# Kernel tuning notes

Measured on AMD Instinct MI355X. Metric: run time of the kernel, lower is better.

Reference implementation:

```python
import jax, jax.numpy as jnp
import numpy as np

HEADS = 16
HEAD_DIM = 64
EMB = HEADS * HEAD_DIM
MAX_REL = 512
B, L = 4, 1024


def _rel_indices(length_q, length_k):
    # Shaw-style clipped relative distance indices into the embeddings table
    dist = jnp.arange(length_k)[None, :] - jnp.arange(length_q)[:, None]
    return jnp.clip(dist, -MAX_REL, MAX_REL) + MAX_REL  # [Lq, Lk] in [0, 2*MAX_REL]


def setup_inputs() -> dict:
    key = jax.random.key(0)
    ks = jax.random.split(key, 16)
    d = {
        "query": jax.random.normal(ks[0], (B, L, EMB), jnp.float32),
        "key": jax.random.normal(ks[1], (B, L, EMB), jnp.float32),
        "value": jax.random.normal(ks[2], (B, L, EMB), jnp.float32),
        "mask": jnp.ones((B, 1, L, L), jnp.int32),
        # per-head Linear(head_dims, head_dims) weights stored torch-style [out, in]
        "Wq": jax.random.normal(ks[3], (HEAD_DIM, HEAD_DIM), jnp.float32) / np.sqrt(HEAD_DIM),
        "bq": jax.random.normal(ks[4], (HEAD_DIM,), jnp.float32) * 0.02,
        "Wk": jax.random.normal(ks[5], (HEAD_DIM, HEAD_DIM), jnp.float32) / np.sqrt(HEAD_DIM),
        "bk": jax.random.normal(ks[6], (HEAD_DIM,), jnp.float32) * 0.02,
        "Wv": jax.random.normal(ks[7], (HEAD_DIM, HEAD_DIM), jnp.float32) / np.sqrt(HEAD_DIM),
        "bv": jax.random.normal(ks[8], (HEAD_DIM,), jnp.float32) * 0.02,
        "Wfc": jax.random.normal(ks[9], (EMB, EMB), jnp.float32) / np.sqrt(EMB),
        "bfc": jax.random.normal(ks[10], (EMB,), jnp.float32) * 0.02,
        "rel_k_table": jax.random.normal(ks[11], (2 * MAX_REL + 1, HEAD_DIM), jnp.float32) * 0.02,
        "rel_v_table": jax.random.normal(ks[12], (2 * MAX_REL + 1, HEAD_DIM), jnp.float32) * 0.02,
    }
    return d


def reference(query, key, value, mask, Wq, bq, Wk, bk, Wv, bv, Wfc, bfc, rel_k_table, rel_v_table):
    b, lq, _ = query.shape
    lk = key.shape[1]
    # split heads then per-head linear projections (torch Linear: x @ W.T + b)
    q = query.reshape(b, lq, HEADS, HEAD_DIM) @ Wq.T + bq
    k = key.reshape(b, lk, HEADS, HEAD_DIM) @ Wk.T + bk
    v = value.reshape(b, lk, HEADS, HEAD_DIM) @ Wv.T + bv

    score = jnp.einsum('bqhd,bkhd->bhqk', q, k)  # [B,H,Lq,Lk]
    score = jnp.where(mask == 0, jnp.float32(-1e20), score)

    idx = _rel_indices(lq, lk)
    a_key = rel_k_table[idx]    # [Lq, Lk, D]
    a_val = rel_v_table[idx]    # [Lq, Lk, D]
    score = score + jnp.einsum('blhd,lrd->bhlr', q, a_key)

    attn = jax.nn.softmax(score / np.sqrt(HEAD_DIM), axis=-1)

    out = jnp.einsum('bhqv,bvhd->bqhd', attn, v)
    # original: einsum('brhl,hld->bhrd', attn[b,h,q,k], a_val[q,k,d]) -> [b,q,h,d]
    out = out + jnp.einsum('bhql,qld->bqhd', attn, a_val)
    out = out.reshape(b, lq, EMB)
    return out @ Wfc.T + bfc
```

## Files before the change

kernel.cpp:

```cpp
#include <hip/hip_runtime.h>
#include <hip/hip_bf16.h>
#include <hip/hip_fp16.h>

#define SEQ 1024
#define HEADS 16
#define HDIM 64
#define EMB 1024
#define TQ 32
#define KQ 256
#define PBA_S 264
#define PBB_S 328
#define RELK_ROWS 1040
#define RELV_S 1064

typedef __bf16 bf16x8 __attribute__((ext_vector_type(8)));
typedef float floatx4 __attribute__((ext_vector_type(4)));

static __device__ __forceinline__ unsigned short f2bu(float f) {
    __bf16 h = (__bf16)f;
    return __builtin_bit_cast(unsigned short, h);
}
static __device__ __forceinline__ float b2f(unsigned short u) {
    unsigned v = ((unsigned)u) << 16;
    return __builtin_bit_cast(float, v);
}

__global__ __launch_bounds__(256) void sa_proj_kernel(
    const float* __restrict__ qin, const float* __restrict__ kin,
    const float* __restrict__ vin,
    const unsigned short* __restrict__ wqb, const unsigned short* __restrict__ wkb,
    const unsigned short* __restrict__ wvb,
    const float* __restrict__ bq, const float* __restrict__ bk,
    const float* __restrict__ bv_,
    unsigned short* __restrict__ qb, unsigned short* __restrict__ kb,
    unsigned short* __restrict__ vtb) {
    const int t = threadIdx.x;
    const int w = t >> 6, lane = t & 63;
    const int quad = lane >> 4, l16 = lane & 15;
    const int which = blockIdx.y;
    const int bx = blockIdx.x;
    const int r0 = (bx >> 2) * 16;
    const int h = (bx & 3) * 4 + w;
    const int bidx = r0 >> 10;
    const int l0 = r0 & 1023;
    const float* x = (which == 0) ? qin : (which == 1) ? kin : vin;
    const unsigned short* Wb = (which == 0) ? wqb : (which == 1) ? wkb : wvb;
    const float* bias = (which == 0) ? bq : (which == 1) ? bk : bv_;

    bf16x8 wf[4][2];
#pragma unroll
    for (int dt = 0; dt < 4; ++dt)
#pragma unroll
        for (int ks = 0; ks < 2; ++ks)
            wf[dt][ks] = *(const bf16x8*)(Wb + (size_t)(dt * 16 + l16) * 64 + ks * 32 + quad * 8);

    bf16x8 xf[2];
#pragma unroll
    for (int ks = 0; ks < 2; ++ks) {
        const float* xp = x + (size_t)(r0 + l16) * EMB + h * 64 + ks * 32 + quad * 8;
        float4 lo = *(const float4*)xp;
        float4 hi = *(const float4*)(xp + 4);
        unsigned short px[8];
        px[0] = f2bu(lo.x); px[1] = f2bu(lo.y); px[2] = f2bu(lo.z); px[3] = f2bu(lo.w);
        px[4] = f2bu(hi.x); px[5] = f2bu(hi.y); px[6] = f2bu(hi.z); px[7] = f2bu(hi.w);
        xf[ks] = *(bf16x8*)px;
    }
    const int bh = bidx * HEADS + h;

    if (which < 2) {
        float biasd[4];
#pragma unroll
        for (int dt = 0; dt < 4; ++dt) biasd[dt] = bias[dt * 16 + l16];
        const float sc = (which == 0) ? 0.125f : 1.0f;
        unsigned short* dst = (which == 0) ? qb : kb;
        floatx4 acc[4];
#pragma unroll
        for (int dt = 0; dt < 4; ++dt) acc[dt] = floatx4{0.f, 0.f, 0.f, 0.f};
#pragma unroll
        for (int dt = 0; dt < 4; ++dt)
#pragma unroll
            for (int ks = 0; ks < 2; ++ks)
                acc[dt] = __builtin_amdgcn_mfma_f32_16x16x32_bf16(xf[ks], wf[dt][ks], acc[dt], 0, 0, 0);
#pragma unroll
        for (int dt = 0; dt < 4; ++dt)
#pragma unroll
            for (int i = 0; i < 4; ++i) {
                const int lr = l0 + quad * 4 + i;
                float val = (acc[dt][i] + biasd[dt]) * sc;
                dst[((size_t)bh * SEQ + lr) * 64 + dt * 16 + l16] = f2bu(val);
            }
    } else {
        float biasv[4][4];
#pragma unroll
        for (int dt = 0; dt < 4; ++dt)
#pragma unroll
            for (int i = 0; i < 4; ++i) biasv[dt][i] = bias[dt * 16 + quad * 4 + i];
        floatx4 acc[4];
#pragma unroll
        for (int dt = 0; dt < 4; ++dt) acc[dt] = floatx4{0.f, 0.f, 0.f, 0.f};
#pragma unroll
        for (int dt = 0; dt < 4; ++dt)
#pragma unroll
            for (int ks = 0; ks < 2; ++ks)
                acc[dt] = __builtin_amdgcn_mfma_f32_16x16x32_bf16(wf[dt][ks], xf[ks], acc[dt], 0, 0, 0);
#pragma unroll
        for (int dt = 0; dt < 4; ++dt)
#pragma unroll
            for (int i = 0; i < 4; ++i) {
                const int d = dt * 16 + quad * 4 + i;
                float val = acc[dt][i] + biasv[dt][i];
                vtb[((size_t)bh * 64 + d) * SEQ + l0 + l16] = f2bu(val);
            }
    }
}

#define NW (1024 * 1024)
#define NRK (RELK_ROWS * 64)
#define NRV (64 * RELV_S)
#define NWP (3 * 4096)
#define CONV_BLOCKS ((NW + NRK + NRV + NWP) / 256)
__global__ __launch_bounds__(256) void sa_prep_kernel(
    const float* __restrict__ Wfc, const float* __restrict__ relk,
    const float* __restrict__ relv,
    const float* __restrict__ Wq, const float* __restrict__ Wk,
    const float* __restrict__ Wv, const int* __restrict__ mask,
    unsigned short* __restrict__ wfcb, unsigned short* __restrict__ relkb,
    unsigned short* __restrict__ relvtb,
    unsigned short* __restrict__ wqb, unsigned short* __restrict__ wkb,
    unsigned short* __restrict__ wvb, unsigned* __restrict__ part) {
    const int bx = blockIdx.x;
    const int t = threadIdx.x;
    if (bx < CONV_BLOCKS) {
        int i = bx * 256 + t;
        if (i < NW) {
            wfcb[i] = f2bu(Wfc[i]);
        } else if (i < NW + NRK) {
            int j = i - NW;
            int r = j >> 6, d = j & 63;
            relkb[j] = (r <= 1024) ? f2bu(relk[r * 64 + d]) : 0;
        } else if (i < NW + NRK + NRV) {
            int j = i - NW - NRK;
            int d = j / RELV_S, c = j - d * RELV_S;
            relvtb[j] = (c <= 1024) ? f2bu(relv[c * 64 + d]) : 0;
        } else {
            int j = i - NW - NRK - NRV;
            int which = j >> 12, e = j & 4095;
            const float* src = (which == 0) ? Wq : (which == 1) ? Wk : Wv;
            unsigned short* dst = (which == 0) ? wqb : (which == 1) ? wkb : wvb;
            dst[e] = f2bu(src[e]);
        }
    } else {
        const int mb = bx - CONV_BLOCKS;
        const int b = mb >> 6, chunk = mb & 63;
        const int4* p = (const int4*)(mask + (size_t)b * (SEQ * SEQ) + chunk * 16384);
        int ok = 1;
#pragma unroll
        for (int i = 0; i < 16; ++i) {
            int4 v = p[t + i * 256];
            ok &= (v.x != 0 && v.y != 0 && v.z != 0 && v.w != 0) ? 1 : 0;
        }
        unsigned long long bal = __ballot(ok);
        __shared__ unsigned wok[4];
        if ((t & 63) == 0) wok[t >> 6] = (bal == ~0ull) ? 1u : 0u;
        __syncthreads();
        if (t == 0)
            part[b * 64 + chunk] = (wok[0] & wok[1] & wok[2] & wok[3]) ? 0xFFFFFFFFu : 0u;
    }
}

__global__ void sa_maskred2(const unsigned* __restrict__ part, unsigned* __restrict__ flags) {
    int t = threadIdx.x;
    if (t < 4) {
        unsigned f = 0xFFFFFFFFu;
        for (int i = 0; i < 64; ++i) f &= part[t * 64 + i];
        flags[t] = f;
    }
}

__global__ __launch_bounds__(512, 8) void sa_attn_kernel(
    const unsigned short* __restrict__ qb, const unsigned short* __restrict__ kb,
    const unsigned short* __restrict__ vtb, const int* __restrict__ mask,
    const unsigned short* __restrict__ relkb, const unsigned short* __restrict__ relvtb,
    const unsigned* __restrict__ flags, __half* __restrict__ Opart,
    float2* __restrict__ ms) {
    __shared__ __align__(16) unsigned short PbA[TQ * PBA_S];
    __shared__ __align__(16) unsigned short PbB[TQ * PBB_S];
    __shared__ float wred[3][TQ * 8];

    const int tid = threadIdx.x;
    const int w = tid >> 6, lane = tid & 63;
    const int quad = lane >> 4, l16 = lane & 15;
    const int bid = blockIdx.x;
    const int quarter = bid & 3;
    const int qt = (bid >> 2) & 31;
    const int bh = bid >> 7;
    const int q0 = qt * TQ;
    const int k0 = quarter * KQ;
    const int b = bh >> 4;
    const bool mfull = (flags[b] == 0xFFFFFFFFu);

    const int cmin = min(512, max(-512, k0 - (q0 + 31))) + 512;
    const int cmax = min(512, max(-512, k0 + 255 - q0)) + 512;
    const int rsb = cmin & ~15;
    const int cb0 = cmin & ~7;

    bf16x8 aq[2][2];
#pragma unroll
    for (int rt = 0; rt < 2; ++rt) {
        const unsigned short* qrow = qb + ((size_t)bh * SEQ + q0 + rt * 16 + l16) * 64;
        aq[rt][0] = *(const bf16x8*)(qrow + quad * 8);
        aq[rt][1] = *(const bf16x8*)(qrow + 32 + quad * 8);
    }

    {
        const int ct_lo = cmin >> 4, ct_hi = cmax >> 4;
        for (int ct = ct_lo + w; ct <= ct_hi; ct += 8) {
            bf16x8 bf0 = *(const bf16x8*)(relkb + (size_t)(ct * 16 + l16) * 64 + quad * 8);
            bf16x8 bf1 = *(const bf16x8*)(relkb + (size_t)(ct * 16 + l16) * 64 + 32 + quad * 8);
            floatx4 r0 = {0.f, 0.f, 0.f, 0.f}, r1 = {0.f, 0.f, 0.f, 0.f};
            r0 = __builtin_amdgcn_mfma_f32_16x16x32_bf16(aq[0][0], bf0, r0, 0, 0, 0);
            r0 = __builtin_amdgcn_mfma_f32_16x16x32_bf16(aq[0][1], bf1, r0, 0, 0, 0);
            r1 = __builtin_amdgcn_mfma_f32_16x16x32_bf16(aq[1][0], bf0, r1, 0, 0, 0);
            r1 = __builtin_amdgcn_mfma_f32_16x16x32_bf16(aq[1][1], bf1, r1, 0, 0, 0);
            const int rcol = ct * 16 + l16;
            if (rcol <= cmax) {
#pragma unroll
                for (int i = 0; i < 4; ++i) {
                    PbB[(quad * 4 + i) * PBB_S + (rcol - rsb)] = f2bu(r0[i]);
                    PbB[(16 + quad * 4 + i) * PBB_S + (rcol - rsb)] = f2bu(r1[i]);
                }
            }
        }
    }
    __syncthreads();

    const int kc = w;
    floatx4 acc[2][2];
#pragma unroll
    for (int rt = 0; rt < 2; ++rt)
#pragma unroll
        for (int tt = 0; tt < 2; ++tt) acc[rt][tt] = floatx4{0.f, 0.f, 0.f, 0.f};
#pragma unroll
    for (int tt = 0; tt < 2; ++tt) {
        const unsigned short* krow = kb + ((size_t)bh * SEQ + k0 + kc * 32 + tt * 16 + l16) * 64;
        bf16x8 kf0 = *(const bf16x8*)(krow + quad * 8);
        bf16x8 kf1 = *(const bf16x8*)(krow + 32 + quad * 8);
        acc[0][tt] = __builtin_amdgcn_mfma_f32_16x16x32_bf16(aq[0][0], kf0, acc[0][tt], 0, 0, 0);
        acc[0][tt] = __builtin_amdgcn_mfma_f32_16x16x32_bf16(aq[0][1], kf1, acc[0][tt], 0, 0, 0);
        acc[1][tt] = __builtin_amdgcn_mfma_f32_16x16x32_bf16(aq[1][0], kf0, acc[1][tt], 0, 0, 0);
        acc[1][tt] = __builtin_amdgcn_mfma_f32_16x16x32_bf16(aq[1][1], kf1, acc[1][tt], 0, 0, 0);
    }
    float rmax[2][4];
#pragma unroll
    for (int rt = 0; rt < 2; ++rt)
#pragma unroll
        for (int i = 0; i < 4; ++i) rmax[rt][i] = -3.0e38f;
    if (mfull) {
#pragma unroll
        for (int rt = 0; rt < 2; ++rt)
#pragma unroll
            for (int tt = 0; tt < 2; ++tt) {
                const int k = k0 + kc * 32 + tt * 16 + l16;
#pragma unroll
                for (int i = 0; i < 4; ++i) {
                    const int row = rt * 16 + quad * 4 + i;
                    const int q = q0 + row;
                    int r = min(512, max(-512, k - q)) + 512;
                    float s = acc[rt][tt][i] + b2f(PbB[row * PBB_S + (r - rsb)]);
                    acc[rt][tt][i] = s;
                    rmax[rt][i] = fmaxf(rmax[rt][i], s);
                }
            }
    } else {
#pragma unroll
        for (int rt = 0; rt < 2; ++rt)
#pragma unroll
            for (int tt = 0; tt < 2; ++tt) {
                const int k = k0 + kc * 32 + tt * 16 + l16;
#pragma unroll
                for (int i = 0; i < 4; ++i) {
                    const int row = rt * 16 + quad * 4 + i;
                    const int q = q0 + row;
                    int r = min(512, max(-512, k - q)) + 512;
                    float s = acc[rt][tt][i] + b2f(PbB[row * PBB_S + (r - rsb)]);
                    int m = mask[(size_t)b * (SEQ * SEQ) + (size_t)q * SEQ + k];
                    s = (m == 0) ? -1e20f : s;
                    acc[rt][tt][i] = s;
                    rmax[rt][i] = fmaxf(rmax[rt][i], s);
                }
            }
    }
#pragma unroll
    for (int rt = 0; rt < 2; ++rt)
#pragma unroll
        for (int i = 0; i < 4; ++i) {
#pragma unroll
            for (int o = 1; o < 16; o <<= 1)
                rmax[rt][i] = fmaxf(rmax[rt][i], __shfl_xor(rmax[rt][i], o));
        }
    if (l16 == 0) {
#pragma unroll
        for (int rt = 0; rt < 2; ++rt)
#pragma unroll
            for (int i = 0; i < 4; ++i)
                wred[0][(rt * 16 + quad * 4 + i) * 8 + kc] = rmax[rt][i];
    }
    __syncthreads();

    if (tid < TQ) {
        float m = wred[0][tid * 8];
#pragma unroll
        for (int j = 1; j < 8; ++j) m = fmaxf(m, wred[0][tid * 8 + j]);
        wred[0][tid * 8] = m;
    }
    for (int g = tid; g < TQ * (PBB_S / 8); g += 512) {
        int row = g / (PBB_S / 8), j = g - row * (PBB_S / 8);
        *(uint4*)&PbB[row * PBB_S + j * 8] = make_uint4(0u, 0u, 0u, 0u);
    }
    __syncthreads();

    float mxr[2][4];
#pragma unroll
    for (int rt = 0; rt < 2; ++rt)
#pragma unroll
        for (int i = 0; i < 4; ++i)
            mxr[rt][i] = wred[0][(rt * 16 + quad * 4 + i) * 8];
    float ssum[2][4] = {{0.f, 0.f, 0.f, 0.f}, {0.f, 0.f, 0.f, 0.f}};
    float tail[2][4] = {{0.f, 0.f, 0.f, 0.f}, {0.f, 0.f, 0.f, 0.f}};
#pragma unroll
    for (int rt = 0; rt < 2; ++rt)
#pragma unroll
        for (int tt = 0; tt < 2; ++tt) {
            const int k = k0 + kc * 32 + tt * 16 + l16;
#pragma unroll
            for (int i = 0; i < 4; ++i) {
                const int row = rt * 16 + quad * 4 + i;
                const int q = q0 + row;
                float p = __expf(acc[rt][tt][i] - mxr[rt][i]);
                ssum[rt][i] += p;
                const int c = k - q + 512;
                const bool interior = ((unsigned)(c - 1) < 1023u);
                tail[rt][i] += interior ? 0.f : p;
                unsigned short pv = f2bu(p);
                PbA[row * PBA_S + (k - k0)] = pv;
                if (interior) PbB[row * PBB_S + (c - cb0)] = pv;
            }
        }
#pragma unroll
    for (int rt = 0; rt < 2; ++rt)
#pragma unroll
        for (int i = 0; i < 4; ++i) {
#pragma unroll
            for (int o = 1; o < 16; o <<= 1) {
                ssum[rt][i] += __shfl_xor(ssum[rt][i], o);
                tail[rt][i] += __shfl_xor(tail[rt][i], o);
            }
        }
    if (l16 == 0) {
#pragma unroll
        for (int rt = 0; rt < 2; ++rt)
#pragma unroll
            for (int i = 0; i < 4; ++i) {
                const int row = rt * 16 + quad * 4 + i;
                wred[1][row * 8 + kc] = ssum[rt][i];
                wred[2][row * 8 + kc] = tail[rt][i];
            }
    }
    __syncthreads();
    if (tid < TQ) {
        float s = 0.f, t = 0.f;
#pragma unroll
        for (int j = 0; j < 8; ++j) {
            s += wred[1][tid * 8 + j];
            t += wred[2][tid * 8 + j];
        }
        const int q = q0 + tid;
        wred[0][tid * 8 + 1] = (q >= k0 + 512) ? t : 0.f;
        wred[0][tid * 8 + 2] = (q <= k0 - 257) ? t : 0.f;
        const int R = bh * SEQ + q;
        ms[(size_t)R * 4 + quarter] = make_float2(wred[0][tid * 8], s);
    }
    __syncthreads();

    {
        const int rt = w & 1;
        const int dq = w >> 1;
        floatx4 accA = {0.f, 0.f, 0.f, 0.f};
        floatx4 accB = {0.f, 0.f, 0.f, 0.f};
        const unsigned short* vbase = vtb + ((size_t)bh * 64 + dq * 16 + l16) * SEQ + k0;
        const unsigned short* rbase = relvtb + (size_t)(dq * 16 + l16) * RELV_S;
#pragma unroll
        for (int it = 0; it < 8; ++it) {
            const int co = it * 32 + quad * 8;
            bf16x8 ap = *(const bf16x8*)&PbA[(rt * 16 + l16) * PBA_S + co];
            bf16x8 bv = *(const bf16x8*)(vbase + co);
            accA = __builtin_amdgcn_mfma_f32_16x16x32_bf16(ap, bv, accA, 0, 0, 0);
        }
        const int nksB = ((cmax - cb0) >> 5) + 1;
        for (int ks = 0; ks < nksB; ++ks) {
            const int co = ks * 32 + quad * 8;
            bf16x8 ar = *(const bf16x8*)&PbB[(rt * 16 + l16) * PBB_S + co];
            bf16x8 br = *(const bf16x8*)(rbase + cb0 + co);
            accB = __builtin_amdgcn_mfma_f32_16x16x32_bf16(ar, br, accB, 0, 0, 0);
        }
        const float rv0 = b2f(rbase[0]);
        const float rv1 = b2f(rbase[1024]);
#pragma unroll
        for (int i = 0; i < 4; ++i) {
            const int row = rt * 16 + quad * 4 + i;
            const int R = bh * SEQ + q0 + row;
            float val = accA[i] + accB[i] +
                        wred[0][row * 8 + 1] * rv0 + wred[0][row * 8 + 2] * rv1;
            Opart[((size_t)R * 4 + quarter) * 64 + dq * 16 + l16] = __float2half(val);
        }
    }
}

__global__ __launch_bounds__(256) void sa_combine_kernel(
    const __half* __restrict__ Opart, const float2* __restrict__ ms,
    unsigned short* __restrict__ aob) {
    const int tid = threadIdx.x;
    const int R = blockIdx.x * 4 + (tid >> 6);
    const int d = tid & 63;
    float2 s[4];
#pragma unroll
    for (int j = 0; j < 4; ++j) s[j] = ms[(size_t)R * 4 + j];
    float m = fmaxf(fmaxf(s[0].x, s[1].x), fmaxf(s[2].x, s[3].x));
    float a[4], denom = 0.f;
#pragma unroll
    for (int j = 0; j < 4; ++j) {
        a[j] = __expf(s[j].x - m);
        denom += s[j].y * a[j];
    }
    float inv = 1.f / denom;
    float val = 0.f;
#pragma unroll
    for (int j = 0; j < 4; ++j)
        val += __half2float(Opart[((size_t)R * 4 + j) * 64 + d]) * a[j];
    val *= inv;
    const int bh = R >> 10, q = R & 1023, b = bh >> 4, h = bh & 15;
    aob[((size_t)b * SEQ + q) * EMB + h * 64 + d] = f2bu(val);
}

__global__ __launch_bounds__(256, 2) void sa_fc_kernel(
    const unsigned short* __restrict__ A, const unsigned short* __restrict__ W,
    const float* __restrict__ bias, float* __restrict__ out) {
    const int t = threadIdx.x;
    const int w = t >> 6, lane = t & 63;
    const int quad = lane >> 4, l16 = lane & 15;
    const int mw = blockIdx.x * 64 + (w & 1) * 32;
    const int nw = blockIdx.y * 256 + (w >> 1) * 128;

    floatx4 acc[2][8];
#pragma unroll
    for (int mt = 0; mt < 2; ++mt)
#pragma unroll
        for (int j = 0; j < 8; ++j) acc[mt][j] = floatx4{0.f, 0.f, 0.f, 0.f};
    float bj[8];
#pragma unroll
    for (int j = 0; j < 8; ++j) bj[j] = bias[nw + j * 16 + l16];

    for (int ks = 0; ks < 32; ++ks) {
        const int co = ks * 32 + quad * 8;
        bf16x8 af0 = *(const bf16x8*)(A + (size_t)(mw + l16) * EMB + co);
        bf16x8 af1 = *(const bf16x8*)(A + (size_t)(mw + 16 + l16) * EMB + co);
#pragma unroll
        for (int j = 0; j < 8; ++j) {
            bf16x8 bf = *(const bf16x8*)(W + (size_t)(nw + j * 16 + l16) * EMB + co);
            acc[0][j] = __builtin_amdgcn_mfma_f32_16x16x32_bf16(af0, bf, acc[0][j], 0, 0, 0);
            acc[1][j] = __builtin_amdgcn_mfma_f32_16x16x32_bf16(af1, bf, acc[1][j], 0, 0, 0);
        }
    }
#pragma unroll
    for (int mt = 0; mt < 2; ++mt)
#pragma unroll
        for (int j = 0; j < 8; ++j) {
            const int col = nw + j * 16 + l16;
#pragma unroll
            for (int i = 0; i < 4; ++i) {
                const size_t row = mw + mt * 16 + quad * 4 + i;
                out[row * EMB + col] = acc[mt][j][i] + bj[j];
            }
        }
}

extern "C" void kernel_launch(void* const* d_in, const int* in_sizes, int n_in,
                              void* d_out, int out_size, void* d_ws, size_t ws_size,
                              hipStream_t stream) {
    const float* query = (const float*)d_in[0];
    const float* key = (const float*)d_in[1];
    const float* value = (const float*)d_in[2];
    const int* mask = (const int*)d_in[3];
    const float* Wq = (const float*)d_in[4];
    const float* bq = (const float*)d_in[5];
    const float* Wk = (const float*)d_in[6];
    const float* bk = (const float*)d_in[7];
    const float* Wv = (const float*)d_in[8];
    const float* bv = (const float*)d_in[9];
    const float* Wfc = (const float*)d_in[10];
    const float* bfc = (const float*)d_in[11];
    const float* relk = (const float*)d_in[12];
    const float* relv = (const float*)d_in[13];
    float* out = (float*)d_out;

    char* base = (char*)d_ws;
    const size_t MB = (size_t)1 << 20;
    unsigned short* qb = (unsigned short*)(base + 0 * MB);
    unsigned short* aob = qb;
    unsigned short* kb = (unsigned short*)(base + 8 * MB);
    unsigned short* vtb = (unsigned short*)(base + 16 * MB);
    unsigned short* wfcb = (unsigned short*)(base + 24 * MB);
    unsigned short* relkb = (unsigned short*)(base + 26 * MB);
    unsigned short* relvtb = (unsigned short*)(base + 26 * MB + 163840);
    unsigned short* wqb = (unsigned short*)(base + 26 * MB + 327680);
    unsigned short* wkb = (unsigned short*)(base + 26 * MB + 335872);
    unsigned short* wvb = (unsigned short*)(base + 26 * MB + 344064);
    unsigned* flags = (unsigned*)(base + 26 * MB + 360448);
    unsigned* part = (unsigned*)(base + 26 * MB + 364544);
    float2* ms = (float2*)(base + 27 * MB);
    __half* Opart = (__half*)(base + 29 * MB);

    sa_prep_kernel<<<CONV_BLOCKS + 256, 256, 0, stream>>>(
        Wfc, relk, relv, Wq, Wk, Wv, mask, wfcb, relkb, relvtb, wqb, wkb, wvb, part);
    sa_proj_kernel<<<dim3(1024, 3), 256, 0, stream>>>(
        query, key, value, wqb, wkb, wvb, bq, bk, bv, qb, kb, vtb);
    sa_maskred2<<<1, 64, 0, stream>>>(part, flags);
    sa_attn_kernel<<<64 * 32 * 4, 512, 0, stream>>>(
        qb, kb, vtb, mask, relkb, relvtb, flags, Opart, ms);
    sa_combine_kernel<<<(4 * HEADS * SEQ) / 4, 256, 0, stream>>>(Opart, ms, aob);
    sa_fc_kernel<<<dim3(64, 4), 256, 0, stream>>>(aob, wfcb, bfc, out);
}
```

Measured before the change: 406.8 us.

## Transpose score MFMA layout, fold log2e into Q, compute row sums via MFMA

Swaps the MFMA operand order so each lane holds a full query row, letting the rel-K bias and probability tiles be written and read as packed 4-wide vectors. This also reduces the row-max reduction to two cross-quad shuffles. Log2(e) is folded into the Q scale so exp2 replaces exp, and a specialized path for unclipped tiles drops the clamp. The separate sum/tail reduction pass and one barrier are replaced by extra MFMAs against a ones vector. Those row sums now come from bf16-rounded probabilities, which slightly changes numerics, and the extra MFMAs add compute.

```diff
diff --git a/kernel.cpp b/kernel.cpp
--- a/kernel.cpp
+++ b/kernel.cpp
@@ -15,6 +15,15 @@
 
 typedef __bf16 bf16x8 __attribute__((ext_vector_type(8)));
 typedef float floatx4 __attribute__((ext_vector_type(4)));
+typedef unsigned short u16x4 __attribute__((ext_vector_type(4)));
+
+#if __has_builtin(__builtin_amdgcn_exp2f)
+#define EXP2F(x) __builtin_amdgcn_exp2f(x)
+#else
+#define EXP2F(x) exp2f(x)
+#endif
+
+#define QSCALE 0.18033688011112042f
 
 static __device__ __forceinline__ unsigned short f2bu(float f) {
     __bf16 h = (__bf16)f;
@@ -71,7 +80,7 @@
         float biasd[4];
 #pragma unroll
         for (int dt = 0; dt < 4; ++dt) biasd[dt] = bias[dt * 16 + l16];
-        const float sc = (which == 0) ? 0.125f : 1.0f;
+        const float sc = (which == 0) ? QSCALE : 1.0f;
         unsigned short* dst = (which == 0) ? qb : kb;
         floatx4 acc[4];
 #pragma unroll
@@ -185,7 +194,8 @@
     float2* __restrict__ ms) {
     __shared__ __align__(16) unsigned short PbA[TQ * PBA_S];
     __shared__ __align__(16) unsigned short PbB[TQ * PBB_S];
-    __shared__ float wred[3][TQ * 8];
+    __shared__ float mxpart[8 * TQ];
+    __shared__ float mxS[TQ];
 
     const int tid = threadIdx.x;
     const int w = tid >> 6, lane = tid & 63;
@@ -198,6 +208,7 @@
     const int k0 = quarter * KQ;
     const int b = bh >> 4;
     const bool mfull = (flags[b] == 0xFFFFFFFFu);
+    const bool clipped = (k0 - (q0 + 31) < -512) || (k0 + 255 - q0 > 512);
 
     const int cmin = min(512, max(-512, k0 - (q0 + 31))) + 512;
     const int cmax = min(512, max(-512, k0 + 255 - q0)) + 512;
@@ -218,23 +229,22 @@
             bf16x8 bf0 = *(const bf16x8*)(relkb + (size_t)(ct * 16 + l16) * 64 + quad * 8);
             bf16x8 bf1 = *(const bf16x8*)(relkb + (size_t)(ct * 16 + l16) * 64 + 32 + quad * 8);
             floatx4 r0 = {0.f, 0.f, 0.f, 0.f}, r1 = {0.f, 0.f, 0.f, 0.f};
-            r0 = __builtin_amdgcn_mfma_f32_16x16x32_bf16(aq[0][0], bf0, r0, 0, 0, 0);
-            r0 = __builtin_amdgcn_mfma_f32_16x16x32_bf16(aq[0][1], bf1, r0, 0, 0, 0);
-            r1 = __builtin_amdgcn_mfma_f32_16x16x32_bf16(aq[1][0], bf0, r1, 0, 0, 0);
-            r1 = __builtin_amdgcn_mfma_f32_16x16x32_bf16(aq[1][1], bf1, r1, 0, 0, 0);
-            const int rcol = ct * 16 + l16;
-            if (rcol <= cmax) {
-#pragma unroll
-                for (int i = 0; i < 4; ++i) {
-                    PbB[(quad * 4 + i) * PBB_S + (rcol - rsb)] = f2bu(r0[i]);
-                    PbB[(16 + quad * 4 + i) * PBB_S + (rcol - rsb)] = f2bu(r1[i]);
-                }
-            }
+            r0 = __builtin_amdgcn_mfma_f32_16x16x32_bf16(bf0, aq[0][0], r0, 0, 0, 0);
+            r0 = __builtin_amdgcn_mfma_f32_16x16x32_bf16(bf1, aq[0][1], r0, 0, 0, 0);
+            r1 = __builtin_amdgcn_mfma_f32_16x16x32_bf16(bf0, aq[1][0], r1, 0, 0, 0);
+            r1 = __builtin_amdgcn_mfma_f32_16x16x32_bf16(bf1, aq[1][1], r1, 0, 0, 0);
+            const int co = ct * 16 + quad * 4 - rsb;
+            u16x4 p0, p1;
+#pragma unroll
+            for (int i = 0; i < 4; ++i) { p0[i] = f2bu(r0[i]); p1[i] = f2bu(r1[i]); }
+            *(u16x4*)&PbB[(size_t)l16 * PBB_S + co] = p0;
+            *(u16x4*)&PbB[(size_t)(16 + l16) * PBB_S + co] = p1;
         }
     }
     __syncthreads();
 
     const int kc = w;
+    const int qg[2] = {q0 + l16, q0 + 16 + l16};
     floatx4 acc[2][2];
 #pragma unroll
     for (int rt = 0; rt < 2; ++rt)
@@ -245,73 +255,82 @@
         const unsigned short* krow = kb + ((size_t)bh * SEQ + k0 + kc * 32 + tt * 16 + l16) * 64;
         bf16x8 kf0 = *(const bf16x8*)(krow + quad * 8);
         bf16x8 kf1 = *(const bf16x8*)(krow + 32 + quad * 8);
-        acc[0][tt] = __builtin_amdgcn_mfma_f32_16x16x32_bf16(aq[0][0], kf0, acc[0][tt], 0, 0, 0);
-        acc[0][tt] = __builtin_amdgcn_mfma_f32_16x16x32_bf16(aq[0][1], kf1, acc[0][tt], 0, 0, 0);
-        acc[1][tt] = __builtin_amdgcn_mfma_f32_16x16x32_bf16(aq[1][0], kf0, acc[1][tt], 0, 0, 0);
-        acc[1][tt] = __builtin_amdgcn_mfma_f32_16x16x32_bf16(aq[1][1], kf1, acc[1][tt], 0, 0, 0);
-    }
-    float rmax[2][4];
-#pragma unroll
-    for (int rt = 0; rt < 2; ++rt)
-#pragma unroll
-        for (int i = 0; i < 4; ++i) rmax[rt][i] = -3.0e38f;
+        acc[0][tt] = __builtin_amdgcn_mfma_f32_16x16x32_bf16(kf0, aq[0][0], acc[0][tt], 0, 0, 0);
+        acc[0][tt] = __builtin_amdgcn_mfma_f32_16x16x32_bf16(kf1, aq[0][1], acc[0][tt], 0, 0, 0);
+        acc[1][tt] = __builtin_amdgcn_mfma_f32_16x16x32_bf16(kf0, aq[1][0], acc[1][tt], 0, 0, 0);
+        acc[1][tt] = __builtin_amdgcn_mfma_f32_16x16x32_bf16(kf1, aq[1][1], acc[1][tt], 0, 0, 0);
+    }
+    float rmax2[2] = {-3.0e38f, -3.0e38f};
     if (mfull) {
-#pragma unroll
-        for (int rt = 0; rt < 2; ++rt)
-#pragma unroll
-            for (int tt = 0; tt < 2; ++tt) {
-                const int k = k0 + kc * 32 + tt * 16 + l16;
+        if (!clipped) {
+#pragma unroll
+            for (int rt = 0; rt < 2; ++rt) {
+                const unsigned short* rsrow = &PbB[(size_t)(rt * 16 + l16) * PBB_S];
+                const int cb = k0 + kc * 32 - qg[rt] + 512 - rsb;
+#pragma unroll
+                for (int tt = 0; tt < 2; ++tt)
+#pragma unroll
+                    for (int i = 0; i < 4; ++i) {
+                        float s = acc[rt][tt][i] + b2f(rsrow[cb + tt * 16 + quad * 4 + i]);
+                        acc[rt][tt][i] = s;
+                        rmax2[rt] = fmaxf(rmax2[rt], s);
+                    }
+            }
+        } else {
+#pragma unroll
+            for (int rt = 0; rt < 2; ++rt) {
+                const unsigned short* rsrow = &PbB[(size_t)(rt * 16 + l16) * PBB_S];
+                const int cb = k0 + kc * 32 - qg[rt] + 512;
+#pragma unroll
+                for (int tt = 0; tt < 2; ++tt)
+#pragma unroll
+                    for (int i = 0; i < 4; ++i) {
+                        const int c = cb + tt * 16 + quad * 4 + i;
+                        const int r = min(1024, max(0, c));
+                        float s = acc[rt][tt][i] + b2f(rsrow[r - rsb]);
+                        acc[rt][tt][i] = s;
+                        rmax2[rt] = fmaxf(rmax2[rt], s);
+                    }
+            }
+        }
+    } else {
+#pragma unroll
+        for (int rt = 0; rt < 2; ++rt) {
+            const unsigned short* rsrow = &PbB[(size_t)(rt * 16 + l16) * PBB_S];
+            const int q = qg[rt];
+            const int cb = k0 + kc * 32 - q + 512;
+            const int* mrow = mask + (size_t)b * (SEQ * SEQ) + (size_t)q * SEQ;
+#pragma unroll
+            for (int tt = 0; tt < 2; ++tt)
 #pragma unroll
                 for (int i = 0; i < 4; ++i) {
-                    const int row = rt * 16 + quad * 4 + i;
-                    const int q = q0 + row;
-                    int r = min(512, max(-512, k - q)) + 512;
-                    float s = acc[rt][tt][i] + b2f(PbB[row * PBB_S + (r - rsb)]);
-                    acc[rt][tt][i] = s;
-                    rmax[rt][i] = fmaxf(rmax[rt][i], s);
-                }
-            }
-    } else {
-#pragma unroll
-        for (int rt = 0; rt < 2; ++rt)
-#pragma unroll
-            for (int tt = 0; tt < 2; ++tt) {
-                const int k = k0 + kc * 32 + tt * 16 + l16;
-#pragma unroll
-                for (int i = 0; i < 4; ++i) {
-                    const int row = rt * 16 + quad * 4 + i;
-                    const int q = q0 + row;
-                    int r = min(512, max(-512, k - q)) + 512;
-                    float s = acc[rt][tt][i] + b2f(PbB[row * PBB_S + (r - rsb)]);
-                    int m = mask[(size_t)b * (SEQ * SEQ) + (size_t)q * SEQ + k];
+                    const int k = k0 + kc * 32 + tt * 16 + quad * 4 + i;
+                    const int c = cb + tt * 16 + quad * 4 + i;
+                    const int r = min(1024, max(0, c));
+                    float s = acc[rt][tt][i] + b2f(rsrow[r - rsb]);
+                    int m = mrow[k];
                     s = (m == 0) ? -1e20f : s;
                     acc[rt][tt][i] = s;
-                    rmax[rt][i] = fmaxf(rmax[rt][i], s);
+                    rmax2[rt] = fmaxf(rmax2[rt], s);
                 }
-            }
-    }
-#pragma unroll
-    for (int rt = 0; rt < 2; ++rt)
-#pragma unroll
-        for (int i = 0; i < 4; ++i) {
-#pragma unroll
-            for (int o = 1; o < 16; o <<= 1)
-                rmax[rt][i] = fmaxf(rmax[rt][i], __shfl_xor(rmax[rt][i], o));
-        }
-    if (l16 == 0) {
-#pragma unroll
-        for (int rt = 0; rt < 2; ++rt)
-#pragma unroll
-            for (int i = 0; i < 4; ++i)
-                wred[0][(rt * 16 + quad * 4 + i) * 8 + kc] = rmax[rt][i];
+        }
+    }
+#pragma unroll
+    for (int rt = 0; rt < 2; ++rt) {
+        rmax2[rt] = fmaxf(rmax2[rt], __shfl_xor(rmax2[rt], 16));
+        rmax2[rt] = fmaxf(rmax2[rt], __shfl_xor(rmax2[rt], 32));
+    }
+    if (quad == 0) {
+        mxpart[kc * 32 + l16] = rmax2[0];
+        mxpart[kc * 32 + 16 + l16] = rmax2[1];
     }
     __syncthreads();
 
     if (tid < TQ) {
-        float m = wred[0][tid * 8];
-#pragma unroll
-        for (int j = 1; j < 8; ++j) m = fmaxf(m, wred[0][tid * 8 + j]);
-        wred[0][tid * 8] = m;
+        float m = mxpart[tid];
+#pragma unroll
+        for (int j = 1; j < 8; ++j) m = fmaxf(m, mxpart[j * 32 + tid]);
+        mxS[tid] = m;
     }
     for (int g = tid; g < TQ * (PBB_S / 8); g += 512) {
         int row = g / (PBB_S / 8), j = g - row * (PBB_S / 8);
@@ -319,66 +338,33 @@
     }
     __syncthreads();
 
-    float mxr[2][4];
-#pragma unroll
-    for (int rt = 0; rt < 2; ++rt)
-#pragma unroll
-        for (int i = 0; i < 4; ++i)
-            mxr[rt][i] = wred[0][(rt * 16 + quad * 4 + i) * 8];
-    float ssum[2][4] = {{0.f, 0.f, 0.f, 0.f}, {0.f, 0.f, 0.f, 0.f}};
-    float tail[2][4] = {{0.f, 0.f, 0.f, 0.f}, {0.f, 0.f, 0.f, 0.f}};
-#pragma unroll
-    for (int rt = 0; rt < 2; ++rt)
-#pragma unroll
-        for (int tt = 0; tt < 2; ++tt) {
-            const int k = k0 + kc * 32 + tt * 16 + l16;
-#pragma unroll
-            for (int i = 0; i < 4; ++i) {
-                const int row = rt * 16 + quad * 4 + i;
-                const int q = q0 + row;
-                float p = __expf(acc[rt][tt][i] - mxr[rt][i]);
-                ssum[rt][i] += p;
-                const int c = k - q + 512;
-                const bool interior = ((unsigned)(c - 1) < 1023u);
-                tail[rt][i] += interior ? 0.f : p;
-                unsigned short pv = f2bu(p);
-                PbA[row * PBA_S + (k - k0)] = pv;
-                if (interior) PbB[row * PBB_S + (c - cb0)] = pv;
-            }
-        }
-#pragma unroll
-    for (int rt = 0; rt < 2; ++rt)
-#pragma unroll
-        for (int i = 0; i < 4; ++i) {
-#pragma unroll
-            for (int o = 1; o < 16; o <<= 1) {
-                ssum[rt][i] += __shfl_xor(ssum[rt][i], o);
-                tail[rt][i] += __shfl_xor(tail[rt][i], o);
-            }
-        }
-    if (l16 == 0) {
-#pragma unroll
-        for (int rt = 0; rt < 2; ++rt)
-#pragma unroll
-            for (int i = 0; i < 4; ++i) {
-                const int row = rt * 16 + quad * 4 + i;
-                wred[1][row * 8 + kc] = ssum[rt][i];
-                wred[2][row * 8 + kc] = tail[rt][i];
-            }
-    }
-    __syncthreads();
-    if (tid < TQ) {
-        float s = 0.f, t = 0.f;
-#pragma unroll
-        for (int j = 0; j < 8; ++j) {
-            s += wred[1][tid * 8 + j];
-            t += wred[2][tid * 8 + j];
-        }
-        const int q = q0 + tid;
-        wred[0][tid * 8 + 1] = (q >= k0 + 512) ? t : 0.f;
-        wred[0][tid * 8 + 2] = (q <= k0 - 257) ? t : 0.f;
-        const int R = bh * SEQ + q;
-        ms[(size_t)R * 4 + quarter] = make_float2(wred[0][tid * 8], s);
+    {
+        const float mxv[2] = {mxS[l16], mxS[16 + l16]};
+#pragma unroll
+        for (int rt = 0; rt < 2; ++rt) {
+            unsigned short* parow = &PbA[(size_t)(rt * 16 + l16) * PBA_S + kc * 32];
+            unsigned short* pbrow = &PbB[(size_t)(rt * 16 + l16) * PBB_S];
+            const int cbase = k0 + kc * 32 - qg[rt] + 512;
+#pragma unroll
+            for (int tt = 0; tt < 2; ++tt) {
+                u16x4 pk;
+#pragma unroll
+                for (int i = 0; i < 4; ++i)
+                    pk[i] = f2bu(EXP2F(acc[rt][tt][i] - mxv[rt]));
+                *(u16x4*)(parow + tt * 16 + quad * 4) = pk;
+                const int c0 = cbase + tt * 16 + quad * 4;
+                if (!clipped) {
+#pragma unroll
+                    for (int i = 0; i < 4; ++i) pbrow[c0 + i - cb0] = pk[i];
+                } else {
+#pragma unroll
+                    for (int i = 0; i < 4; ++i) {
+                        const int c = c0 + i;
+                        if ((unsigned)(c - 1) < 1023u) pbrow[c - cb0] = pk[i];
+                    }
+                }
+            }
+        }
     }
     __syncthreads();
 
@@ -387,31 +373,50 @@
         const int dq = w >> 1;
         floatx4 accA = {0.f, 0.f, 0.f, 0.f};
         floatx4 accB = {0.f, 0.f, 0.f, 0.f};
+        floatx4 accS = {0.f, 0.f, 0.f, 0.f};
+        floatx4 accSI = {0.f, 0.f, 0.f, 0.f};
+        unsigned short ob[8];
+#pragma unroll
+        for (int j = 0; j < 8; ++j) ob[j] = 0x3F80;
+        const bf16x8 onesf = *(bf16x8*)ob;
         const unsigned short* vbase = vtb + ((size_t)bh * 64 + dq * 16 + l16) * SEQ + k0;
         const unsigned short* rbase = relvtb + (size_t)(dq * 16 + l16) * RELV_S;
 #pragma unroll
         for (int it = 0; it < 8; ++it) {
             const int co = it * 32 + quad * 8;
-            bf16x8 ap = *(const bf16x8*)&PbA[(rt * 16 + l16) * PBA_S + co];
+            bf16x8 ap = *(const bf16x8*)&PbA[(size_t)(rt * 16 + l16) * PBA_S + co];
             bf16x8 bv = *(const bf16x8*)(vbase + co);
             accA = __builtin_amdgcn_mfma_f32_16x16x32_bf16(ap, bv, accA, 0, 0, 0);
+            accS = __builtin_amdgcn_mfma_f32_16x16x32_bf16(ap, onesf, accS, 0, 0, 0);
         }
         const int nksB = ((cmax - cb0) >> 5) + 1;
         for (int ks = 0; ks < nksB; ++ks) {
             const int co = ks * 32 + quad * 8;
-            bf16x8 ar = *(const bf16x8*)&PbB[(rt * 16 + l16) * PBB_S + co];
+            bf16x8 ar = *(const bf16x8*)&PbB[(size_t)(rt * 16 + l16) * PBB_S + co];
             bf16x8 br = *(const bf16x8*)(rbase + cb0 + co);
             accB = __builtin_amdgcn_mfma_f32_16x16x32_bf16(ar, br, accB, 0, 0, 0);
+            accSI = __builtin_amdgcn_mfma_f32_16x16x32_bf16(ar, onesf, accSI, 0, 0, 0);
         }
         const float rv0 = b2f(rbase[0]);
         const float rv1 = b2f(rbase[1024]);
 #pragma unroll
         for (int i = 0; i < 4; ++i) {
             const int row = rt * 16 + quad * 4 + i;
-            const int R = bh * SEQ + q0 + row;
-            float val = accA[i] + accB[i] +
-                        wred[0][row * 8 + 1] * rv0 + wred[0][row * 8 + 2] * rv1;
+            const int q = q0 + row;
+            const float tail = accS[i] - accSI[i];
+            const float lowS = (q >= k0 + 512) ? tail : 0.f;
+            const float highS = (q <= k0 - 257) ? tail : 0.f;
+            const int R = bh * SEQ + q;
+            float val = accA[i] + accB[i] + lowS * rv0 + highS * rv1;
             Opart[((size_t)R * 4 + quarter) * 64 + dq * 16 + l16] = __float2half(val);
+        }
+        if (dq == 0 && l16 == 0) {
+#pragma unroll
+            for (int i = 0; i < 4; ++i) {
+                const int row = rt * 16 + quad * 4 + i;
+                ms[(size_t)(bh * SEQ + q0 + row) * 4 + quarter] =
+                    make_float2(mxS[row], accS[i]);
+            }
         }
     }
 }
@@ -429,7 +434,7 @@
     float a[4], denom = 0.f;
 #pragma unroll
     for (int j = 0; j < 4; ++j) {
-        a[j] = __expf(s[j].x - m);
+        a[j] = EXP2F(s[j].x - m);
         denom += s[j].y * a[j];
     }
     float inv = 1.f / denom;
```

Measured after the change: 397.5 us. 2.3% less time.
